# Performance work log

Measured on AMD Instinct MI355X. Metric: run time of the kernel, lower is better.

## Reference

```python
import jax, jax.numpy as jnp
import numpy as np

H = 2048
N = 2_097_152
BINS = 256


def _tensor2image(x):
    # de-normalize from [-1,1]-style to [0,1] (SCGAN's tensor2image)
    return x * 0.5 + 0.5


def _cdf(vals):
    # torch.histc(vals, bins=256, min=0, max=256): unit-width bins; values here lie in [0,256)
    b = jnp.clip(jnp.floor(vals), 0, BINS - 1).astype(jnp.int32)
    hist = jnp.zeros((BINS,), jnp.float32).at[b].add(1.0)
    c = jnp.cumsum(hist)
    return c / c[BINS - 1]


def _trans_table(ref_cdf, adj_cdf):
    # table[i] = first j in 1..255 with adj[j-1] <= ref[i] <= adj[j]; else i. table[0]=0, table[255]=255.
    r = ref_cdf[:, None]                # [256,1]
    lo = adj_cdf[None, :-1]             # adj[j-1], j=1..255
    hi = adj_cdf[None, 1:]              # adj[j]
    cond = (lo <= r) & (r <= hi)        # [256,255]
    found = jnp.any(cond, axis=1)
    j_first = 1 + jnp.argmax(cond, axis=1)
    table = jnp.where(found, j_first, jnp.arange(BINS))
    table = table.at[0].set(0).at[BINS - 1].set(BINS - 1)
    return table


def _histogram_matching(dst_img, ref_img, i0, i1, i2, i3):
    dst_align = dst_img[:, i0, i1]      # [3,N]
    ref_align = ref_img[:, i2, i3]      # [3,N]
    cdf_dst = jax.vmap(_cdf)(dst_align)           # [3,256]
    cdf_ref = jax.vmap(_cdf)(ref_align)           # [3,256]
    tables = jax.vmap(_trans_table)(cdf_dst, cdf_ref)  # [3,256] int
    ix = jnp.clip(jnp.floor(dst_align), 0, BINS - 1).astype(jnp.int32)
    matched = jnp.take_along_axis(tables, ix, axis=1).astype(dst_img.dtype)  # [3,N]
    return dst_img.at[:, i0, i1].set(matched)


def setup_inputs() -> dict:
    key = jax.random.key(0)
    ks = jax.random.split(key, 9)
    return {
        "input_data": jax.random.uniform(ks[0], (1, 3, H, H), jnp.float32),
        "target_data": jax.random.uniform(ks[1], (1, 3, H, H), jnp.float32),
        "mask_src": jax.random.randint(ks[2], (1, 1, H, H), 0, 2).astype(jnp.float32),
        "mask_tar": jax.random.randint(ks[3], (1, 1, H, H), 0, 2).astype(jnp.float32),
        "idx0": jax.random.randint(ks[4], (N,), 0, H),
        "idx1": jax.random.randint(ks[5], (N,), 0, H),
        "idx2": jax.random.randint(ks[6], (N,), 0, H),
        "idx3": jax.random.randint(ks[7], (N,), 0, H),
        "ref": jax.random.uniform(ks[8], (1, 3, H, H), jnp.float32),
    }


def reference(input_data, target_data, mask_src, mask_tar, idx0, idx1, idx2, idx3, ref):
    img = _tensor2image(input_data)[0] * 255.0   # [3,H,H]
    tgt = _tensor2image(target_data)[0] * 255.0  # [3,H,H]
    rf = _tensor2image(ref)[0] * 255.0           # [3,H,H]
    m_src = jnp.broadcast_to(mask_src[0, 0], img.shape)
    m_tar = jnp.broadcast_to(mask_tar[0, 0], tgt.shape)
    input_masked = img * m_src
    target_masked = tgt * m_tar
    ref_masked = rf * m_src
    match = jax.lax.stop_gradient(
        _histogram_matching(ref_masked, target_masked, idx0, idx1, idx2, idx3)
    ) * m_src
    return jnp.mean(jnp.abs(input_masked - match))
```

## Files before the change

### kernel.cpp

```cpp
#include <hip/hip_runtime.h>

#define H 2048
#define HH (H * H)
#define NIDX 2097152
#define BINS 256
#define CH 3

#define NLIST 128
#define CAPG  139264
#define WS_HIST_DST 0
#define WS_HIST_REF 3072
#define WS_TABLE    6144
#define WS_ACC      9216
#define WS_CURS     9728
#define WS_CTRL_BYTES 16384
#define WS_SEL      16384
#define WS_ZERO_BYTES (16384 + (size_t)HH)
#define WS_BPS      (16384 + (size_t)HH)
#define WS_BPR      (WS_BPS + (size_t)HH * 4)
#define WS_LIST     (WS_BPR + (size_t)HH * 4)
#define WS_MAIN_BYTES (WS_LIST + (size_t)NLIST * CAPG * 2)

#define FB_CNT_DST  16384
#define FB_BINPACK  (16384 + (size_t)HH * 2)
#define FB_ZERO_BYTES (16384 + (size_t)HH * 2)

__device__ __forceinline__ int bin_of(float v) {
    int b = (int)floorf(v);
    return min(max(b, 0), BINS - 1);
}



#define P1_BLOCKS 512
#define P1_SPB (NIDX / P1_BLOCKS)
#define P1_CAP 96
#define FUSE_GRID (P1_BLOCKS + 2048)

__global__ __launch_bounds__(256) void prep_part_kernel(
    const float* __restrict__ mask_src, const float* __restrict__ mask_tar,
    const float* __restrict__ refimg, const float* __restrict__ tgtimg,
    unsigned int* __restrict__ bps, unsigned int* __restrict__ bpr,
    const int* __restrict__ idx0, const int* __restrict__ idx1,
    const int* __restrict__ idx2, const int* __restrict__ idx3,
    unsigned short* __restrict__ list_g, unsigned int* __restrict__ curs)
{
    __shared__ unsigned short stage[NLIST * P1_CAP];
    __shared__ unsigned int lcnt[NLIST];
    __shared__ unsigned int lbase[NLIST];

    if (blockIdx.x < P1_BLOCKS) {
        for (int i = threadIdx.x; i < NLIST; i += 256) lcnt[i] = 0u;
        __syncthreads();

        const int base4 = blockIdx.x * (P1_SPB / 4);
        #pragma unroll
        for (int r = 0; r < P1_SPB / 1024; ++r) {
            int k4 = base4 + r * 256 + threadIdx.x;
            int4 a = ((const int4*)idx0)[k4];
            int4 b = ((const int4*)idx1)[k4];
            int4 c = ((const int4*)idx2)[k4];
            int4 d = ((const int4*)idx3)[k4];
            const int pd[4] = { a.x * H + b.x, a.y * H + b.y,
                                a.z * H + b.z, a.w * H + b.w };
            const int pr[4] = { c.x * H + d.x, c.y * H + d.y,
                                c.z * H + d.z, c.w * H + d.w };
            #pragma unroll
            for (int e = 0; e < 4; ++e) {
                {
                    int l = pd[e] >> 16;
                    unsigned int pos = atomicAdd(&lcnt[l], 1u);
                    if (pos < P1_CAP) stage[l * P1_CAP + pos] = (unsigned short)(pd[e] & 0xFFFF);
                    else {
                        unsigned int g = atomicAdd(&curs[l], 1u);
                        if (g < CAPG) list_g[(size_t)l * CAPG + g] = (unsigned short)(pd[e] & 0xFFFF);
                    }
                }
                {
                    int l = 64 + (pr[e] >> 16);
                    unsigned int pos = atomicAdd(&lcnt[l], 1u);
                    if (pos < P1_CAP) stage[l * P1_CAP + pos] = (unsigned short)(pr[e] & 0xFFFF);
                    else {
                        unsigned int g = atomicAdd(&curs[l], 1u);
                        if (g < CAPG) list_g[(size_t)l * CAPG + g] = (unsigned short)(pr[e] & 0xFFFF);
                    }
                }
            }
        }
        __syncthreads();
        if (threadIdx.x < NLIST) {
            unsigned int n = min(lcnt[threadIdx.x], (unsigned int)P1_CAP);
            lbase[threadIdx.x] = atomicAdd(&curs[threadIdx.x], n);
        }
        __syncthreads();
        const int wave = threadIdx.x >> 6;
        const int lane = threadIdx.x & 63;
        for (int b = wave; b < NLIST; b += 4) {
            int n = (int)min(lcnt[b], (unsigned int)P1_CAP);
            unsigned int gb = lbase[b];
            for (int e = lane; e < n; e += 64) {
                unsigned int gi = gb + e;
                if (gi < CAPG) list_g[(size_t)b * CAPG + gi] = stage[b * P1_CAP + e];
            }
        }
    } else {
        const int t = (int)(blockIdx.x - P1_BLOCKS) * 256 + threadIdx.x;
        const int q = t << 1;
        float4 msA = ((const float4*)mask_src)[q];
        float4 msB = ((const float4*)mask_src)[q + 1];
        float4 mtA = ((const float4*)mask_tar)[q];
        float4 mtB = ((const float4*)mask_tar)[q + 1];
        const float ms[8] = { msA.x, msA.y, msA.z, msA.w, msB.x, msB.y, msB.z, msB.w };
        const float mt[8] = { mtA.x, mtA.y, mtA.z, mtA.w, mtB.x, mtB.y, mtB.z, mtB.w };
        unsigned int wsrc[8] = { 0u,0u,0u,0u,0u,0u,0u,0u };
        unsigned int wref[8] = { 0u,0u,0u,0u,0u,0u,0u,0u };
        #pragma unroll
        for (int c = 0; c < CH; ++c) {
            float4 rA = ((const float4*)(refimg + (size_t)c * HH))[q];
            float4 rB = ((const float4*)(refimg + (size_t)c * HH))[q + 1];
            float4 tA = ((const float4*)(tgtimg + (size_t)c * HH))[q];
            float4 tB = ((const float4*)(tgtimg + (size_t)c * HH))[q + 1];
            const float rr[8] = { rA.x, rA.y, rA.z, rA.w, rB.x, rB.y, rB.z, rB.w };
            const float tt[8] = { tA.x, tA.y, tA.z, tA.w, tB.x, tB.y, tB.z, tB.w };
            #pragma unroll
            for (int e = 0; e < 8; ++e) {
                float vs = (rr[e] * 0.5f + 0.5f) * 255.0f * ms[e];
                float vt = (tt[e] * 0.5f + 0.5f) * 255.0f * mt[e];
                wsrc[e] |= ((unsigned int)bin_of(vs)) << (8 * c);
                wref[e] |= ((unsigned int)bin_of(vt)) << (8 * c);
            }
        }
        uint4 s1 = { wsrc[0], wsrc[1], wsrc[2], wsrc[3] };
        uint4 s2 = { wsrc[4], wsrc[5], wsrc[6], wsrc[7] };
        uint4 r1 = { wref[0], wref[1], wref[2], wref[3] };
        uint4 r2 = { wref[4], wref[5], wref[6], wref[7] };
        ((uint4*)bps)[q]     = s1;
        ((uint4*)bps)[q + 1] = s2;
        ((uint4*)bpr)[q]     = r1;
        ((uint4*)bpr)[q + 1] = r2;
    }
}

__global__ __launch_bounds__(256) void gather_hist_kernel(
    const unsigned short* __restrict__ list_g, const unsigned int* __restrict__ curs,
    const unsigned int* __restrict__ bps, const unsigned int* __restrict__ bpr,
    unsigned char* __restrict__ selected,
    unsigned int* __restrict__ hist_dst, unsigned int* __restrict__ hist_ref)
{
    __shared__ unsigned int hh[CH * BINS];
    for (int i = threadIdx.x; i < CH * BINS; i += 256) hh[i] = 0u;
    __syncthreads();

    const int xcd  = blockIdx.x & 7;
    const int j    = blockIdx.x >> 3;
    const int bsl  = j & 15;
    const int sub  = j >> 4;
    const int side = bsl >> 3;
    const int bucket = xcd * 8 + (bsl & 7);
    const int l = side * 64 + bucket;
    const unsigned int pbase = ((unsigned int)bucket) << 16;
    const unsigned int* __restrict__ src = side ? bpr : bps;

    const unsigned int n = min(curs[l], (unsigned int)CAPG);
    const unsigned int chunk = (((n + 15u) >> 4) + 7u) & ~7u;
    const unsigned int s = (unsigned int)sub * chunk;
    const unsigned int e = min(s + chunk, n);
    const unsigned short* lbase = list_g + (size_t)l * CAPG;

    unsigned int zc = 0;
    for (unsigned int ib = s + (unsigned int)threadIdx.x * 8u; ib < e; ib += 2048u) {
        unsigned int w[8];
        unsigned int pcnt;
        if (ib + 8u <= e) {
            uint4 raw = *(const uint4*)(lbase + ib);
            const unsigned int ent[8] = {
                raw.x & 0xFFFFu, raw.x >> 16, raw.y & 0xFFFFu, raw.y >> 16,
                raw.z & 0xFFFFu, raw.z >> 16, raw.w & 0xFFFFu, raw.w >> 16 };
            #pragma unroll
            for (int k = 0; k < 8; ++k) {
                unsigned int p = pbase | ent[k];
                w[k] = src[p];
                if (side == 0) selected[p] = 1;
            }
            pcnt = 8u;
        } else {
            pcnt = e - ib;
            #pragma unroll
            for (int k = 0; k < 8; ++k) {
                if ((unsigned int)k < pcnt) {
                    unsigned int p = pbase | (unsigned int)lbase[ib + k];
                    w[k] = src[p];
                    if (side == 0) selected[p] = 1;
                } else w[k] = 0xFFFFFFFFu;
            }
        }
        #pragma unroll
        for (int k = 0; k < 8; ++k) {
            if ((unsigned int)k < pcnt) {
                unsigned int ww = w[k];
                if (ww == 0u) ++zc;
                else {
                    atomicAdd(&hh[0 * BINS + (ww & 0xFFu)], 1u);
                    atomicAdd(&hh[1 * BINS + ((ww >> 8) & 0xFFu)], 1u);
                    atomicAdd(&hh[2 * BINS + ((ww >> 16) & 0xFFu)], 1u);
                }
            }
        }
    }

    int z = (int)zc;
    #pragma unroll
    for (int off = 32; off; off >>= 1) z += __shfl_down(z, off);
    if ((threadIdx.x & 63) == 0 && z) {
        atomicAdd(&hh[0 * BINS], (unsigned int)z);
        atomicAdd(&hh[1 * BINS], (unsigned int)z);
        atomicAdd(&hh[2 * BINS], (unsigned int)z);
    }

    __syncthreads();
    unsigned int* dsthist = side ? hist_ref : hist_dst;
    for (int i = threadIdx.x; i < CH * BINS; i += 256) {
        unsigned int v = hh[i];
        if (v) atomicAdd(&dsthist[i], v);
    }
}

__global__ __launch_bounds__(256) void table_kernel(
    const unsigned int* __restrict__ hist_dst,
    const unsigned int* __restrict__ hist_ref,
    int* __restrict__ table)
{
    __shared__ float cd[CH * BINS];
    __shared__ float cr[CH * BINS];
    __shared__ float wpart[4];
    const int i = threadIdx.x;
    const int lane = i & 63;
    const int wave = i >> 6;

    for (int a = 0; a < 6; ++a) {
        const unsigned int* h = (a < 3) ? (hist_dst + a * BINS) : (hist_ref + (a - 3) * BINS);
        float* out = (a < 3) ? (cd + a * BINS) : (cr + (a - 3) * BINS);
        float x = (float)h[i];
        #pragma unroll
        for (int off = 1; off < 64; off <<= 1) {
            float y = __shfl_up(x, off);
            if (lane >= off) x += y;
        }
        if (lane == 63) wpart[wave] = x;
        __syncthreads();
        float prefix = 0.0f;
        #pragma unroll
        for (int w = 0; w < 3; ++w) if (w < wave) prefix += wpart[w];
        x += prefix;
        float tot = wpart[0] + wpart[1] + wpart[2] + wpart[3];
        out[i] = x / tot;
        __syncthreads();
    }

    #pragma unroll
    for (int c = 0; c < CH; ++c) {
        int t;
        if (i == 0) t = 0;
        else if (i == BINS - 1) t = BINS - 1;
        else {
            float r = cd[c * BINS + i];
            int lo = 1, hi = BINS - 1;
            while (lo < hi) {
                int mid = (lo + hi) >> 1;
                if (cr[c * BINS + mid] < r) lo = mid + 1; else hi = mid;
            }
            t = (cr[c * BINS + lo - 1] <= r) ? lo : i;
        }
        table[c * BINS + i] = t;
    }
}

__global__ __launch_bounds__(256) void loss_sel_kernel(
    const float* __restrict__ input, const float* __restrict__ refimg,
    const float* __restrict__ mask_src, const unsigned char* __restrict__ selected,
    const int* __restrict__ table, double* __restrict__ acc)
{
    __shared__ int tab[CH * BINS];
    for (int i = threadIdx.x; i < CH * BINS; i += 256) tab[i] = table[i];
    __syncthreads();

    const int t = blockIdx.x * 256 + threadIdx.x;
    const int q = t << 1;
    float4 mA = ((const float4*)mask_src)[q];
    float4 mB = ((const float4*)mask_src)[q + 1];
    uchar4 sA = ((const uchar4*)selected)[q];
    uchar4 sB = ((const uchar4*)selected)[q + 1];
    const unsigned char ss[8] = { sA.x, sA.y, sA.z, sA.w, sB.x, sB.y, sB.z, sB.w };
    const float mm[8] = { mA.x, mA.y, mA.z, mA.w, mB.x, mB.y, mB.z, mB.w };

    float lsum = 0.0f;
    #pragma unroll
    for (int c = 0; c < CH; ++c) {
        float4 aA = ((const float4*)(input + (size_t)c * HH))[q];
        float4 aB = ((const float4*)(input + (size_t)c * HH))[q + 1];
        float4 rA = ((const float4*)(refimg + (size_t)c * HH))[q];
        float4 rB = ((const float4*)(refimg + (size_t)c * HH))[q + 1];
        const float aa[8] = { aA.x, aA.y, aA.z, aA.w, aB.x, aB.y, aB.z, aB.w };
        const float rr[8] = { rA.x, rA.y, rA.z, rA.w, rB.x, rB.y, rB.z, rB.w };
        #pragma unroll
        for (int e = 0; e < 8; ++e) {
            float m = mm[e];
            float av = (aa[e] * 0.5f + 0.5f) * 255.0f * m;
            float rv = (rr[e] * 0.5f + 0.5f) * 255.0f * m;
            float tv = (float)tab[c * BINS + bin_of(rv)];
            float mv = m * (ss[e] ? tv : rv);
            lsum += fabsf(av - mv);
        }
    }

    double d = (double)lsum;
    #pragma unroll
    for (int off = 32; off; off >>= 1) d += __shfl_down(d, off);
    __shared__ double wsum[4];
    int wid = threadIdx.x >> 6;
    int lane = threadIdx.x & 63;
    if (lane == 0) wsum[wid] = d;
    __syncthreads();
    if (threadIdx.x == 0) {
        double tt = wsum[0] + wsum[1] + wsum[2] + wsum[3];
        atomicAdd(acc, tt);
    }
}

__global__ void finalize_kernel(const double* __restrict__ acc, float* __restrict__ out)
{
    if (threadIdx.x == 0 && blockIdx.x == 0) {
        out[0] = (float)(acc[0] / (double)(CH * (double)HH));
    }
}


__device__ __forceinline__ void cnt_inc(unsigned int* cnt, int p) {
    atomicAdd(&cnt[p >> 1], (p & 1) ? 0x10000u : 1u);
}

__global__ __launch_bounds__(256) void fb_prep_kernel(
    const float* __restrict__ mask_tar, const float* __restrict__ tgtimg,
    unsigned int* __restrict__ binpack)
{
    const int nq = HH / 4;
    const int stride = gridDim.x * 256;
    for (int q = blockIdx.x * 256 + threadIdx.x; q < nq; q += stride) {
        float4 m4 = ((const float4*)mask_tar)[q];
        const float mm[4] = { m4.x, m4.y, m4.z, m4.w };
        unsigned int w[4] = { 0u, 0u, 0u, 0u };
        #pragma unroll
        for (int c = 0; c < CH; ++c) {
            float4 t4 = ((const float4*)(tgtimg + (size_t)c * HH))[q];
            const float tt[4] = { t4.x, t4.y, t4.z, t4.w };
            #pragma unroll
            for (int e = 0; e < 4; ++e) {
                float v = (tt[e] * 0.5f + 0.5f) * 255.0f * mm[e];
                w[e] |= ((unsigned int)bin_of(v)) << (8 * c);
            }
        }
        uint4 out = { w[0], w[1], w[2], w[3] };
        ((uint4*)binpack)[q] = out;
    }
}

__global__ __launch_bounds__(256) void fb_scatter_kernel(
    const int4* __restrict__ idx0, const int4* __restrict__ idx1,
    const int4* __restrict__ idx2, const int4* __restrict__ idx3,
    const unsigned int* __restrict__ binpack,
    unsigned int* __restrict__ cnt_dst, unsigned int* __restrict__ hist_ref)
{
    __shared__ unsigned int hr[CH * BINS];
    for (int i = threadIdx.x; i < CH * BINS; i += 256) hr[i] = 0u;
    __syncthreads();

    unsigned int zc = 0;
    const int n4 = NIDX / 4;
    const int stride = gridDim.x * 256;
    for (int k = blockIdx.x * 256 + threadIdx.x; k < n4; k += stride) {
        int4 a = idx0[k], b = idx1[k], c = idx2[k], d = idx3[k];
        int p0 = c.x * H + d.x, p1 = c.y * H + d.y;
        int p2 = c.z * H + d.z, p3 = c.w * H + d.w;
        unsigned int w0 = binpack[p0], w1 = binpack[p1];
        unsigned int w2 = binpack[p2], w3 = binpack[p3];

        cnt_inc(cnt_dst, a.x * H + b.x);
        cnt_inc(cnt_dst, a.y * H + b.y);
        cnt_inc(cnt_dst, a.z * H + b.z);
        cnt_inc(cnt_dst, a.w * H + b.w);

        const unsigned int ws2[4] = { w0, w1, w2, w3 };
        #pragma unroll
        for (int e = 0; e < 4; ++e) {
            unsigned int w = ws2[e];
            if (w == 0u) ++zc;
            else {
                atomicAdd(&hr[0 * BINS + (w & 0xFFu)], 1u);
                atomicAdd(&hr[1 * BINS + ((w >> 8) & 0xFFu)], 1u);
                atomicAdd(&hr[2 * BINS + ((w >> 16) & 0xFFu)], 1u);
            }
        }
    }

    int z = (int)zc;
    #pragma unroll
    for (int off = 32; off; off >>= 1) z += __shfl_down(z, off);
    if ((threadIdx.x & 63) == 0 && z) {
        atomicAdd(&hr[0 * BINS], (unsigned int)z);
        atomicAdd(&hr[1 * BINS], (unsigned int)z);
        atomicAdd(&hr[2 * BINS], (unsigned int)z);
    }

    __syncthreads();
    for (int i = threadIdx.x; i < CH * BINS; i += 256) {
        unsigned int v = hr[i];
        if (v) atomicAdd(&hist_ref[i], v);
    }
}

__global__ __launch_bounds__(256) void fb_sweep_kernel(
    const float* __restrict__ mask_src, const float* __restrict__ refimg,
    const unsigned int* __restrict__ cnt_dst,
    unsigned int* __restrict__ hist_dst)
{
    __shared__ unsigned int hd[CH * BINS];
    for (int i = threadIdx.x; i < CH * BINS; i += 256) hd[i] = 0u;
    __syncthreads();

    unsigned int zc = 0;
    const int nq = HH / 4;
    const int stride = gridDim.x * 256;
    for (int q = blockIdx.x * 256 + threadIdx.x; q < nq; q += stride) {
        uint2 wd = ((const uint2*)cnt_dst)[q];
        unsigned int cdc[4] = { wd.x & 0xFFFFu, wd.x >> 16, wd.y & 0xFFFFu, wd.y >> 16 };
        float4 ms4 = ((const float4*)mask_src)[q];
        const float ms[4] = { ms4.x, ms4.y, ms4.z, ms4.w };

        float rv[CH][4];
        #pragma unroll
        for (int c = 0; c < CH; ++c) {
            float4 r4 = ((const float4*)(refimg + (size_t)c * HH))[q];
            rv[c][0] = r4.x; rv[c][1] = r4.y; rv[c][2] = r4.z; rv[c][3] = r4.w;
        }
        #pragma unroll
        for (int e = 0; e < 4; ++e) {
            if (cdc[e]) {
                if (ms[e] == 0.0f) zc += cdc[e];
                else {
                    #pragma unroll
                    for (int c = 0; c < CH; ++c) {
                        float v = (rv[c][e] * 0.5f + 0.5f) * 255.0f;
                        atomicAdd(&hd[c * BINS + bin_of(v)], cdc[e]);
                    }
                }
            }
        }
    }

    int z = (int)zc;
    #pragma unroll
    for (int off = 32; off; off >>= 1) z += __shfl_down(z, off);
    if ((threadIdx.x & 63) == 0 && z) {
        atomicAdd(&hd[0 * BINS], (unsigned int)z);
        atomicAdd(&hd[1 * BINS], (unsigned int)z);
        atomicAdd(&hd[2 * BINS], (unsigned int)z);
    }

    __syncthreads();
    for (int i = threadIdx.x; i < CH * BINS; i += 256) {
        unsigned int v = hd[i];
        if (v) atomicAdd(&hist_dst[i], v);
    }
}

__global__ __launch_bounds__(256) void fb_loss_kernel(
    const float* __restrict__ input, const float* __restrict__ refimg,
    const float* __restrict__ mask_src, const unsigned int* __restrict__ cnt_dst,
    const int* __restrict__ table, double* __restrict__ acc)
{
    __shared__ int tab[CH * BINS];
    for (int i = threadIdx.x; i < CH * BINS; i += 256) tab[i] = table[i];
    __syncthreads();

    float lsum = 0.0f;
    const int nq = HH / 4;
    const int stride = gridDim.x * 256;
    for (int q = blockIdx.x * 256 + threadIdx.x; q < nq; q += stride) {
        float4 m4 = ((const float4*)mask_src)[q];
        uint2 w = ((const uint2*)cnt_dst)[q];
        const unsigned int sel[4] = { w.x & 0xFFFFu, w.x >> 16, w.y & 0xFFFFu, w.y >> 16 };
        const float mm[4] = { m4.x, m4.y, m4.z, m4.w };
        #pragma unroll
        for (int c = 0; c < CH; ++c) {
            float4 a4 = ((const float4*)(input + (size_t)c * HH))[q];
            float4 r4 = ((const float4*)(refimg + (size_t)c * HH))[q];
            const float aa[4] = { a4.x, a4.y, a4.z, a4.w };
            const float rr[4] = { r4.x, r4.y, r4.z, r4.w };
            #pragma unroll
            for (int e = 0; e < 4; ++e) {
                float m = mm[e];
                float av = (aa[e] * 0.5f + 0.5f) * 255.0f * m;
                float rv = (rr[e] * 0.5f + 0.5f) * 255.0f * m;
                float tv = (float)tab[c * BINS + bin_of(rv)];
                float mv = m * (sel[e] ? tv : rv);
                lsum += fabsf(av - mv);
            }
        }
    }

    double d = (double)lsum;
    #pragma unroll
    for (int off = 32; off; off >>= 1) d += __shfl_down(d, off);
    __shared__ double wsum[4];
    int wid = threadIdx.x >> 6;
    int lane = threadIdx.x & 63;
    if (lane == 0) wsum[wid] = d;
    __syncthreads();
    if (threadIdx.x == 0) {
        double t = wsum[0] + wsum[1] + wsum[2] + wsum[3];
        atomicAdd(acc, t);
    }
}


extern "C" void kernel_launch(void* const* d_in, const int* in_sizes, int n_in,
                              void* d_out, int out_size, void* d_ws, size_t ws_size,
                              hipStream_t stream)
{
    const float* input    = (const float*)d_in[0];
    const float* target   = (const float*)d_in[1];
    const float* mask_src = (const float*)d_in[2];
    const float* mask_tar = (const float*)d_in[3];
    const int*   idx0     = (const int*)d_in[4];
    const int*   idx1     = (const int*)d_in[5];
    const int*   idx2     = (const int*)d_in[6];
    const int*   idx3     = (const int*)d_in[7];
    const float* refimg   = (const float*)d_in[8];

    char* ws = (char*)d_ws;
    unsigned int* hist_dst = (unsigned int*)(ws + WS_HIST_DST);
    unsigned int* hist_ref = (unsigned int*)(ws + WS_HIST_REF);
    int*          table    = (int*)(ws + WS_TABLE);
    double*       acc      = (double*)(ws + WS_ACC);

    if (ws_size >= WS_MAIN_BYTES) {
        unsigned int*   curs     = (unsigned int*)(ws + WS_CURS);
        unsigned char*  selected = (unsigned char*)(ws + WS_SEL);
        unsigned int*   bps      = (unsigned int*)(ws + WS_BPS);
        unsigned int*   bpr      = (unsigned int*)(ws + WS_BPR);
        unsigned short* list_g   = (unsigned short*)(ws + WS_LIST);

        hipMemsetAsync(d_ws, 0, WS_ZERO_BYTES, stream);
        prep_part_kernel<<<FUSE_GRID, 256, 0, stream>>>(
            mask_src, mask_tar, refimg, target, bps, bpr,
            idx0, idx1, idx2, idx3, list_g, curs);
        gather_hist_kernel<<<2048, 256, 0, stream>>>(list_g, curs, bps, bpr,
                                                     selected, hist_dst, hist_ref);
        table_kernel<<<1, 256, 0, stream>>>(hist_dst, hist_ref, table);
        loss_sel_kernel<<<2048, 256, 0, stream>>>(input, refimg, mask_src,
                                                  selected, table, acc);
        finalize_kernel<<<1, 64, 0, stream>>>(acc, (float*)d_out);
    } else {
        unsigned int* cnt_dst = (unsigned int*)(ws + FB_CNT_DST);
        unsigned int* binpack = (unsigned int*)(ws + FB_BINPACK);

        hipMemsetAsync(d_ws, 0, FB_ZERO_BYTES, stream);
        fb_prep_kernel<<<2048, 256, 0, stream>>>(mask_tar, target, binpack);
        fb_scatter_kernel<<<2048, 256, 0, stream>>>((const int4*)idx0, (const int4*)idx1,
                                                    (const int4*)idx2, (const int4*)idx3,
                                                    binpack, cnt_dst, hist_ref);
        fb_sweep_kernel<<<1024, 256, 0, stream>>>(mask_src, refimg, cnt_dst, hist_dst);
        table_kernel<<<1, 256, 0, stream>>>(hist_dst, hist_ref, table);
        fb_loss_kernel<<<2048, 256, 0, stream>>>(input, refimg, mask_src, cnt_dst,
                                                 table, acc);
        finalize_kernel<<<1, 64, 0, stream>>>(acc, (float*)d_out);
    }
}
```

Measured before the change: 302.8 us.

## Fold table build and finalize into last-block tails; rebalance partition blocks

Removes two separate kernel launches: the CDF/table computation now runs in the last finishing block of the gather-histogram kernel, and the final mean runs in the last block of the loss kernel, both detected with an atomic done counter. It also doubles the partition-phase block count and halves the per-block staging capacity. This cuts launch gaps and tail bubbles between tiny kernels, at the cost of extra fences and atomics in every block and a serialized tail in one block.

```diff
diff --git a/kernel.cpp b/kernel.cpp
--- a/kernel.cpp
+++ b/kernel.cpp
@@ -13,6 +13,8 @@
 #define WS_TABLE    6144
 #define WS_ACC      9216
 #define WS_CURS     9728
+#define WS_DONE_G   10240
+#define WS_DONE_L   10244
 #define WS_CTRL_BYTES 16384
 #define WS_SEL      16384
 #define WS_ZERO_BYTES (16384 + (size_t)HH)
@@ -32,9 +34,9 @@
 
 
 
-#define P1_BLOCKS 512
+#define P1_BLOCKS 1024
 #define P1_SPB (NIDX / P1_BLOCKS)
-#define P1_CAP 96
+#define P1_CAP 48
 #define FUSE_GRID (P1_BLOCKS + 2048)
 
 __global__ __launch_bounds__(256) void prep_part_kernel(
@@ -145,7 +147,8 @@
     const unsigned short* __restrict__ list_g, const unsigned int* __restrict__ curs,
     const unsigned int* __restrict__ bps, const unsigned int* __restrict__ bpr,
     unsigned char* __restrict__ selected,
-    unsigned int* __restrict__ hist_dst, unsigned int* __restrict__ hist_ref)
+    unsigned int* __restrict__ hist_dst, unsigned int* __restrict__ hist_ref,
+    int* __restrict__ table, unsigned int* __restrict__ done)
 {
     __shared__ unsigned int hh[CH * BINS];
     for (int i = threadIdx.x; i < CH * BINS; i += 256) hh[i] = 0u;
@@ -223,13 +226,18 @@
         unsigned int v = hh[i];
         if (v) atomicAdd(&dsthist[i], v);
     }
-}
-
-__global__ __launch_bounds__(256) void table_kernel(
-    const unsigned int* __restrict__ hist_dst,
-    const unsigned int* __restrict__ hist_ref,
-    int* __restrict__ table)
-{
+
+    __shared__ int is_last;
+    __syncthreads();
+    if (threadIdx.x == 0) {
+        __threadfence();
+        unsigned int t = atomicAdd(done, 1u);
+        is_last = (t == gridDim.x - 1u) ? 1 : 0;
+    }
+    __syncthreads();
+    if (!is_last) return;
+    __threadfence();
+
     __shared__ float cd[CH * BINS];
     __shared__ float cr[CH * BINS];
     __shared__ float wpart[4];
@@ -238,9 +246,9 @@
     const int wave = i >> 6;
 
     for (int a = 0; a < 6; ++a) {
-        const unsigned int* h = (a < 3) ? (hist_dst + a * BINS) : (hist_ref + (a - 3) * BINS);
+        unsigned int* h = (a < 3) ? (hist_dst + a * BINS) : (hist_ref + (a - 3) * BINS);
         float* out = (a < 3) ? (cd + a * BINS) : (cr + (a - 3) * BINS);
-        float x = (float)h[i];
+        float x = (float)atomicAdd(&h[i], 0u);
         #pragma unroll
         for (int off = 1; off < 64; off <<= 1) {
             float y = __shfl_up(x, off);
@@ -278,7 +286,8 @@
 __global__ __launch_bounds__(256) void loss_sel_kernel(
     const float* __restrict__ input, const float* __restrict__ refimg,
     const float* __restrict__ mask_src, const unsigned char* __restrict__ selected,
-    const int* __restrict__ table, double* __restrict__ acc)
+    const int* __restrict__ table, double* __restrict__ acc,
+    float* __restrict__ out_loss, unsigned int* __restrict__ done)
 {
     __shared__ int tab[CH * BINS];
     for (int i = threadIdx.x; i < CH * BINS; i += 256) tab[i] = table[i];
@@ -324,6 +333,71 @@
     if (threadIdx.x == 0) {
         double tt = wsum[0] + wsum[1] + wsum[2] + wsum[3];
         atomicAdd(acc, tt);
+    }
+
+    __shared__ int is_last;
+    __syncthreads();
+    if (threadIdx.x == 0) {
+        __threadfence();
+        unsigned int tk = atomicAdd(done, 1u);
+        is_last = (tk == gridDim.x - 1u) ? 1 : 0;
+    }
+    __syncthreads();
+    if (!is_last) return;
+    if (threadIdx.x == 0) {
+        __threadfence();
+        double a = atomicAdd(acc, 0.0);
+        out_loss[0] = (float)(a / (double)(CH * (double)HH));
+    }
+}
+
+__global__ __launch_bounds__(256) void table_kernel(
+    const unsigned int* __restrict__ hist_dst,
+    const unsigned int* __restrict__ hist_ref,
+    int* __restrict__ table)
+{
+    __shared__ float cd[CH * BINS];
+    __shared__ float cr[CH * BINS];
+    __shared__ float wpart[4];
+    const int i = threadIdx.x;
+    const int lane = i & 63;
+    const int wave = i >> 6;
+
+    for (int a = 0; a < 6; ++a) {
+        const unsigned int* h = (a < 3) ? (hist_dst + a * BINS) : (hist_ref + (a - 3) * BINS);
+        float* out = (a < 3) ? (cd + a * BINS) : (cr + (a - 3) * BINS);
+        float x = (float)h[i];
+        #pragma unroll
+        for (int off = 1; off < 64; off <<= 1) {
+            float y = __shfl_up(x, off);
+            if (lane >= off) x += y;
+        }
+        if (lane == 63) wpart[wave] = x;
+        __syncthreads();
+        float prefix = 0.0f;
+        #pragma unroll
+        for (int w = 0; w < 3; ++w) if (w < wave) prefix += wpart[w];
+        x += prefix;
+        float tot = wpart[0] + wpart[1] + wpart[2] + wpart[3];
+        out[i] = x / tot;
+        __syncthreads();
+    }
+
+    #pragma unroll
+    for (int c = 0; c < CH; ++c) {
+        int t;
+        if (i == 0) t = 0;
+        else if (i == BINS - 1) t = BINS - 1;
+        else {
+            float r = cd[c * BINS + i];
+            int lo = 1, hi = BINS - 1;
+            while (lo < hi) {
+                int mid = (lo + hi) >> 1;
+                if (cr[c * BINS + mid] < r) lo = mid + 1; else hi = mid;
+            }
+            t = (cr[c * BINS + lo - 1] <= r) ? lo : i;
+        }
+        table[c * BINS + i] = t;
     }
 }
 
@@ -545,6 +619,8 @@
 
     if (ws_size >= WS_MAIN_BYTES) {
         unsigned int*   curs     = (unsigned int*)(ws + WS_CURS);
+        unsigned int*   done_g   = (unsigned int*)(ws + WS_DONE_G);
+        unsigned int*   done_l   = (unsigned int*)(ws + WS_DONE_L);
         unsigned char*  selected = (unsigned char*)(ws + WS_SEL);
         unsigned int*   bps      = (unsigned int*)(ws + WS_BPS);
         unsigned int*   bpr      = (unsigned int*)(ws + WS_BPR);
@@ -555,11 +631,11 @@
             mask_src, mask_tar, refimg, target, bps, bpr,
             idx0, idx1, idx2, idx3, list_g, curs);
         gather_hist_kernel<<<2048, 256, 0, stream>>>(list_g, curs, bps, bpr,
-                                                     selected, hist_dst, hist_ref);
-        table_kernel<<<1, 256, 0, stream>>>(hist_dst, hist_ref, table);
+                                                     selected, hist_dst, hist_ref,
+                                                     table, done_g);
         loss_sel_kernel<<<2048, 256, 0, stream>>>(input, refimg, mask_src,
-                                                  selected, table, acc);
-        finalize_kernel<<<1, 64, 0, stream>>>(acc, (float*)d_out);
+                                                  selected, table, acc,
+                                                  (float*)d_out, done_l);
     } else {
         unsigned int* cnt_dst = (unsigned int*)(ws + FB_CNT_DST);
         unsigned int* binpack = (unsigned int*)(ws + FB_BINPACK);
```

Result: slower. 466.9 us (+54.2%).
